# Performance work log

Hardware: AMD Instinct MI355X
Metric: run time of the kernel (lower is better)

## Reference

```python
import jax, jax.numpy as jnp
import numpy as np

MAX_RHO = 12.0
N_THETAS = 16
N_RHOS = 5
G = N_THETAS * N_RHOS          # 80 gaussians
W_NUM = 5                      # weights_num == n_feat -> per-channel conv
OUT_DIM = 80                   # conv_shape = [80, 80]
EPS = 1e-5


def _initial_coords():
    grid_rho = np.linspace(0.0, MAX_RHO, num=N_RHOS + 1)[1:]
    grid_theta = np.linspace(0.0, 2.0 * np.pi, num=N_THETAS + 1)[:-1]
    gr, gt = np.meshgrid(grid_rho, grid_theta, sparse=False)
    return gr.T.flatten().astype(np.float32), gt.T.flatten().astype(np.float32)


def setup_inputs() -> dict:
    key = jax.random.key(0)
    ks = jax.random.split(key, 6)
    B, N, V = 2, 500, 64
    input_feat = jax.random.normal(ks[0], (B, N, V, W_NUM), dtype=jnp.float32)
    rho_coords = jax.random.uniform(ks[1], (B, N, V), dtype=jnp.float32) * MAX_RHO
    theta_coords = jax.random.uniform(ks[2], (B, N, V), dtype=jnp.float32) * (2.0 * np.pi)
    mask = (jax.random.uniform(ks[3], (B, N, V, 1)) > 0.2).astype(jnp.float32)

    mu_r0, mu_t0 = _initial_coords()
    mu_rho = jnp.tile(jnp.asarray(mu_r0)[None, :], (W_NUM, 1))       # [W, G]
    mu_theta = jnp.tile(jnp.asarray(mu_t0)[None, :], (W_NUM, 1))     # [W, G]
    sigma_rho = jnp.full((W_NUM, G), MAX_RHO / 8.0, dtype=jnp.float32)
    sigma_theta = jnp.ones((W_NUM, G), dtype=jnp.float32)

    # VarianceScaling(scale=1, fan_avg, uniform): limit = sqrt(3 / fan_avg)
    limit = np.sqrt(3.0 / ((G + OUT_DIM) / 2.0)).astype(np.float32)
    W_conv = jax.random.uniform(ks[4], (W_NUM, G, OUT_DIM), dtype=jnp.float32,
                                minval=-limit, maxval=limit)
    b_conv = jnp.zeros((W_NUM, OUT_DIM), dtype=jnp.float32)

    return {
        "input_feat": input_feat, "rho_coords": rho_coords,
        "theta_coords": theta_coords, "mask": mask,
        "mu_rho": mu_rho, "mu_theta": mu_theta,
        "sigma_rho": sigma_rho, "sigma_theta": sigma_theta,
        "W_conv": W_conv, "b_conv": b_conv,
        "n_rotations": 16,
    }


def reference(input_feat, rho_coords, theta_coords, mask,
              mu_rho, mu_theta, sigma_rho, sigma_theta,
              W_conv, b_conv, n_rotations):
    # input_feat: [B,N,V,W]; rho/theta: [B,N,V]; mask: [B,N,V,1]
    two_pi = 2.0 * np.pi
    # rho gaussian is rotation-independent -> compute once: [B,N,V,W,G]
    g_rho = jnp.exp(-jnp.square(rho_coords[..., None, None] - mu_rho)
                    / (jnp.square(sigma_rho) + EPS))
    m = mask[..., None]                      # [B,N,V,1,1]

    def one_rotation(k):
        th = jnp.mod(theta_coords + k * (two_pi / n_rotations), two_pi)
        g_th = jnp.exp(-jnp.square(th[..., None, None] - mu_theta)
                       / (jnp.square(sigma_theta) + EPS))    # [B,N,V,W,G]
        gauss = g_rho * g_th * m
        gauss = gauss / (jnp.sum(gauss, axis=2, keepdims=True) + EPS)  # mean over vertices
        # weighted patch aggregation: each weight i sees only feature channel i
        desc = jnp.einsum('bnvwg,bnvw->bnwg', gauss, input_feat)
        return jnp.einsum('bnwg,wgo->bnwo', desc, W_conv) + b_conv     # [B,N,W,O]

    ks = jnp.arange(n_rotations, dtype=jnp.float32)

    def body(carry, k):
        return jnp.maximum(carry, one_rotation(k)), None

    init = one_rotation(ks[0])
    out, _ = jax.lax.scan(body, init, ks[1:])
    return out  # [B, n_samples, weights_num, conv_shape[0]]
```

## Files before the change

kernel.cpp:

```cpp
#include <hip/hip_runtime.h>

#define V 64
#define W 5
#define G 80
#define O 80
#define NROT 16
#define GPAD 104
#define EPSV 1e-5f
#define NLOG2E (-1.4426950408889634f)

#define XSTR 68

using bf16x8 = __attribute__((ext_vector_type(8))) short;
using f32x4  = __attribute__((ext_vector_type(4))) float;

__device__ __forceinline__ unsigned short f2bf(float x) {
    unsigned u = __float_as_uint(x);
    unsigned r = (u + 0x7FFFu + ((u >> 16) & 1u)) >> 16;
    return (unsigned short)r;
}
__device__ __forceinline__ float pick5(float a0, float a1, float a2,
                                       float a3, float a4, int r) {
    float x = (r == 1) ? a1 : a0;
    x = (r == 2) ? a2 : x;
    x = (r == 3) ? a3 : x;
    x = (r == 4) ? a4 : x;
    return x;
}

#if __has_builtin(__builtin_amdgcn_mfma_f32_16x16x32_f16)
typedef _Float16 elem_t;
typedef elem_t efrag __attribute__((ext_vector_type(8)));
#define EMFMA(a, b, c) __builtin_amdgcn_mfma_f32_16x16x32_f16((a), (b), (c), 0, 0, 0)
__device__ __forceinline__ unsigned epack(float a, float b) {
    auto r = __builtin_amdgcn_cvt_pkrtz(a, b);
    return __builtin_bit_cast(unsigned, r);
}
#else
typedef short elem_t;
typedef elem_t efrag __attribute__((ext_vector_type(8)));
#define EMFMA(a, b, c) __builtin_amdgcn_mfma_f32_16x16x32_bf16((a), (b), (c), 0, 0, 0)
__device__ __forceinline__ unsigned epack(float a, float b) {
    return (unsigned)f2bf(a) | ((unsigned)f2bf(b) << 16);
}
#endif

__global__ __launch_bounds__(64) void pack_wc_kernel(
    const float* __restrict__ Wc, unsigned short* __restrict__ wsB)
{
    const int f = blockIdx.x, l = threadIdx.x;
    const int w = f / 15, r = f % 15, ks = r / 5, nt = r % 5;
    const int g0 = ks * 32 + ((l >> 4) << 3);
    const int o  = nt * 16 + (l & 15);
    unsigned short v[8];
    #pragma unroll
    for (int i = 0; i < 8; ++i) {
        int g = g0 + i;
        v[i] = (g < G) ? f2bf(Wc[(w * G + g) * O + o]) : (unsigned short)0;
    }
    *(uint4*)(wsB + ((size_t)f * 64 + l) * 8) = *(const uint4*)v;
}

__global__ __launch_bounds__(320, 6) void conv_kernel(
    const float* __restrict__ feat,
    const float* __restrict__ rho,
    const float* __restrict__ theta,
    const float* __restrict__ mask,
    const float* __restrict__ mu_rho,
    const float* __restrict__ mu_theta,
    const float* __restrict__ sig_rho,
    const float* __restrict__ sig_theta,
    const unsigned short* __restrict__ wsB,
    const float* __restrict__ bc,
    float* __restrict__ out)
{
    __shared__ __align__(16) float s_x[NROT][XSTR];
    __shared__ __align__(16) float s_fT[W][XSTR];
    __shared__ __align__(16) float s_arg[5][XSTR];
    __shared__ __align__(16) unsigned short s_descT[W * NROT * GPAD];
    __shared__ float s_ct[16], s_mt[16], s_shift[8], s_sre[8];

    const int tid = threadIdx.x;
    const int p = blockIdx.x;
    const int g = tid % G;
    const int j = tid / G;

    const float kstep = 0.39269908169872414f;
    const float two_pi = 6.283185307179586f;
    const float inv_two_pi = 0.15915494309189535f;

    {
        int v = tid / 5, w = tid - 5 * (tid / 5);
        s_fT[w][v] = feat[p * V * W + tid];
    }
    {
        int r = tid >> 6, v = tid & 63;
        float mu_r = mu_rho[r * 16];
        float sr   = sig_rho[r * 16];
        float c_r  = NLOG2E / (sr * sr + EPSV);
        float rv   = rho[p * V + v];
        float mk   = (mask[p * V + v] != 0.0f) ? 0.0f : -1e30f;
        float dr = rv - mu_r;
        float av = fmaf(dr * dr, c_r, mk);
        s_arg[r][v] = av;
        float m = av;
        m = fmaxf(m, __shfl_xor(m, 1));
        m = fmaxf(m, __shfl_xor(m, 2));
        m = fmaxf(m, __shfl_xor(m, 4));
        m = fmaxf(m, __shfl_xor(m, 8));
        m = fmaxf(m, __shfl_xor(m, 16));
        m = fmaxf(m, __shfl_xor(m, 32));
        if (v == 0) {
            float sh = fminf(-m, 60.0f);
            s_shift[r] = sh;
            s_sre[r]   = EPSV * __builtin_amdgcn_exp2f(sh);
        }
    }
    if (tid < 16) {
        float st = sig_theta[tid];
        s_ct[tid] = NLOG2E / (st * st + EPSV);
        s_mt[tid] = mu_theta[tid];
    }
    for (int i = tid; i < V * NROT; i += 320) {
        int v = i >> 4, k = i & 15;
        float x = theta[p * V + v] + (float)k * kstep;
        x -= floorf(x * inv_two_pi) * two_pi;
        s_x[k][v] = x;
    }

    const int wchk = 1 + j;
    const int gr = (g >> 4) << 4;
    const int gt = g & 15;
    int pred = (mu_rho  [wchk * G + g] == mu_rho  [g]) &&
               (mu_theta[wchk * G + g] == mu_theta[g]) &&
               (sig_rho [wchk * G + g] == sig_rho [g]) &&
               (sig_theta[wchk * G + g] == sig_theta[g]) &&
               (mu_rho  [g] == mu_rho  [gr]) &&
               (sig_rho [g] == sig_rho [gr]) &&
               (mu_theta[g] == mu_theta[gt]) &&
               (sig_theta[g] == sig_theta[gt]);
    const int uni = __syncthreads_and(pred);

    if (uni) {
        const int ww = tid >> 6;
        const int l  = tid & 63;
        const int lg = l >> 4, lc = l & 15;
        const int v0 = lg << 3;

        efrag a00, a01, a10, a11;
        {
            int w_a = lc / 5, r_a = lc - 5 * (lc / 5);
            float sh = s_shift[r_a];
            const float* ap = &s_arg[r_a][0];
            const float* fp = &s_fT[w_a][0];
            float4 aa = *(const float4*)(ap + v0);
            float4 ab = *(const float4*)(ap + v0 + 4);
            float4 fa = *(const float4*)(fp + v0);
            float4 fb = *(const float4*)(fp + v0 + 4);
            a00 = __builtin_bit_cast(efrag, make_uint4(
                epack(__builtin_amdgcn_exp2f(aa.x + sh) * fa.x,
                      __builtin_amdgcn_exp2f(aa.y + sh) * fa.y),
                epack(__builtin_amdgcn_exp2f(aa.z + sh) * fa.z,
                      __builtin_amdgcn_exp2f(aa.w + sh) * fa.w),
                epack(__builtin_amdgcn_exp2f(ab.x + sh) * fb.x,
                      __builtin_amdgcn_exp2f(ab.y + sh) * fb.y),
                epack(__builtin_amdgcn_exp2f(ab.z + sh) * fb.z,
                      __builtin_amdgcn_exp2f(ab.w + sh) * fb.w)));
            aa = *(const float4*)(ap + 32 + v0);
            ab = *(const float4*)(ap + 32 + v0 + 4);
            fa = *(const float4*)(fp + 32 + v0);
            fb = *(const float4*)(fp + 32 + v0 + 4);
            a01 = __builtin_bit_cast(efrag, make_uint4(
                epack(__builtin_amdgcn_exp2f(aa.x + sh) * fa.x,
                      __builtin_amdgcn_exp2f(aa.y + sh) * fa.y),
                epack(__builtin_amdgcn_exp2f(aa.z + sh) * fa.z,
                      __builtin_amdgcn_exp2f(aa.w + sh) * fa.w),
                epack(__builtin_amdgcn_exp2f(ab.x + sh) * fb.x,
                      __builtin_amdgcn_exp2f(ab.y + sh) * fb.y),
                epack(__builtin_amdgcn_exp2f(ab.z + sh) * fb.z,
                      __builtin_amdgcn_exp2f(ab.w + sh) * fb.w)));
        }
        if (lc < 14) {
            int m = 16 + lc;
            bool wf = (m < 25);
            int w_b = wf ? (m / 5) : 0;
            int r_b = wf ? (m - 5 * (m / 5)) : (lc - 9);
            float sh = s_shift[r_b];
            const float* ap = &s_arg[r_b][0];
            const float* fp = &s_fT[w_b][0];
            float4 aa = *(const float4*)(ap + v0);
            float4 ab = *(const float4*)(ap + v0 + 4);
            float4 fa = *(const float4*)(fp + v0);
            float4 fb = *(const float4*)(fp + v0 + 4);
            if (!wf) { fa = make_float4(1.f,1.f,1.f,1.f); fb = fa; }
            a10 = __builtin_bit_cast(efrag, make_uint4(
                epack(__builtin_amdgcn_exp2f(aa.x + sh) * fa.x,
                      __builtin_amdgcn_exp2f(aa.y + sh) * fa.y),
                epack(__builtin_amdgcn_exp2f(aa.z + sh) * fa.z,
                      __builtin_amdgcn_exp2f(aa.w + sh) * fa.w),
                epack(__builtin_amdgcn_exp2f(ab.x + sh) * fb.x,
                      __builtin_amdgcn_exp2f(ab.y + sh) * fb.y),
                epack(__builtin_amdgcn_exp2f(ab.z + sh) * fb.z,
                      __builtin_amdgcn_exp2f(ab.w + sh) * fb.w)));
            aa = *(const float4*)(ap + 32 + v0);
            ab = *(const float4*)(ap + 32 + v0 + 4);
            fa = *(const float4*)(fp + 32 + v0);
            fb = *(const float4*)(fp + 32 + v0 + 4);
            if (!wf) { fa = make_float4(1.f,1.f,1.f,1.f); fb = fa; }
            a11 = __builtin_bit_cast(efrag, make_uint4(
                epack(__builtin_amdgcn_exp2f(aa.x + sh) * fa.x,
                      __builtin_amdgcn_exp2f(aa.y + sh) * fa.y),
                epack(__builtin_amdgcn_exp2f(aa.z + sh) * fa.z,
                      __builtin_amdgcn_exp2f(aa.w + sh) * fa.w),
                epack(__builtin_amdgcn_exp2f(ab.x + sh) * fb.x,
                      __builtin_amdgcn_exp2f(ab.y + sh) * fb.y),
                epack(__builtin_amdgcn_exp2f(ab.z + sh) * fb.z,
                      __builtin_amdgcn_exp2f(ab.w + sh) * fb.w)));
        } else {
            uint4 zz = make_uint4(0u, 0u, 0u, 0u);
            a10 = __builtin_bit_cast(efrag, zz);
            a11 = __builtin_bit_cast(efrag, zz);
        }

        const float sre0 = s_sre[0], sre1 = s_sre[1], sre2 = s_sre[2],
                    sre3 = s_sre[3], sre4 = s_sre[4];

        int w0[4], r0[4], w1[4], r1[4];
        bool ok1[4];
        #pragma unroll
        for (int i = 0; i < 4; ++i) {
            int m = lg * 4 + i;
            w0[i] = m / 5; r0[i] = m - 5 * w0[i];
            int m2 = 16 + lg * 4 + i;
            ok1[i] = (m2 < 25);
            int mm = ok1[i] ? m2 : 24;
            w1[i] = mm / 5; r1[i] = mm - 5 * w1[i];
        }

        #pragma unroll
        for (int q = 0; q < 4; ++q) {
            int nt = ww + 5 * q;
            if (nt < 16) {
                float ct = s_ct[nt], mt = s_mt[nt];
                float bco = -2.0f * ct * mt;
                float cco = ct * mt * mt;
                const float* xr = &s_x[lc][v0];
                float4 xa = *(const float4*)(xr);
                float4 xb = *(const float4*)(xr + 4);
                float4 xc = *(const float4*)(xr + 32);
                float4 xd = *(const float4*)(xr + 36);
                #define EX(v) __builtin_amdgcn_exp2f(\
                    fmaf(fmaf(ct, (v), bco), (v), cco))
                efrag b0 = __builtin_bit_cast(efrag, make_uint4(
                    epack(EX(xa.x), EX(xa.y)), epack(EX(xa.z), EX(xa.w)),
                    epack(EX(xb.x), EX(xb.y)), epack(EX(xb.z), EX(xb.w))));
                efrag b1 = __builtin_bit_cast(efrag, make_uint4(
                    epack(EX(xc.x), EX(xc.y)), epack(EX(xc.z), EX(xc.w)),
                    epack(EX(xd.x), EX(xd.y)), epack(EX(xd.z), EX(xd.w))));
                #undef EX

                f32x4 z = {0.f, 0.f, 0.f, 0.f};
                f32x4 c0 = EMFMA(a00, b0, z);
                c0 = EMFMA(a01, b1, c0);
                f32x4 c1 = EMFMA(a10, b0, z);
                c1 = EMFMA(a11, b1, c1);

                float dn0 = __shfl(c1[1], 32 + lc);
                float dn1 = __shfl(c1[2], 32 + lc);
                float dn2 = __shfl(c1[3], 32 + lc);
                float dn3 = __shfl(c1[0], 48 + lc);
                float dn4 = __shfl(c1[1], 48 + lc);
                float i0 = __builtin_amdgcn_rcpf(dn0 + sre0);
                float i1 = __builtin_amdgcn_rcpf(dn1 + sre1);
                float i2 = __builtin_amdgcn_rcpf(dn2 + sre2);
                float i3 = __builtin_amdgcn_rcpf(dn3 + sre3);
                float i4 = __builtin_amdgcn_rcpf(dn4 + sre4);

                #pragma unroll
                for (int i = 0; i < 4; ++i) {
                    float inv = pick5(i0, i1, i2, i3, i4, r0[i]);
                    s_descT[(w0[i] * 16 + lc) * GPAD + r0[i] * 16 + nt] =
                        f2bf(c0[i] * inv);
                }
                #pragma unroll
                for (int i = 0; i < 4; ++i) {
                    if (ok1[i]) {
                        float inv = pick5(i0, i1, i2, i3, i4, r1[i]);
                        s_descT[(w1[i] * 16 + lc) * GPAD + r1[i] * 16 + nt] =
                            f2bf(c1[i] * inv);
                    }
                }
            }
        }
    } else {
        #pragma unroll 1
        for (int w = 0; w < W; ++w) {
            const float mu_r = mu_rho[w * G + g];
            const float sr   = sig_rho[w * G + g];
            const float c_sr = NLOG2E / (sr * sr + EPSV);
            const float mu_t = mu_theta[w * G + g];
            const float st   = sig_theta[w * G + g];
            const float c_st = NLOG2E / (st * st + EPSV);
            float den[4] = {0.f, 0.f, 0.f, 0.f};
            float nm[4]  = {0.f, 0.f, 0.f, 0.f};
            for (int v = 0; v < V; ++v) {
                float rv  = rho[p * V + v];
                float mk  = (mask[p * V + v] != 0.0f) ? 0.0f : -1e30f;
                float fw  = s_fT[w][v];
                float dr = rv - mu_r;
                float argr = fmaf(dr * dr, c_sr, mk);
                #pragma unroll
                for (int kk = 0; kk < 4; ++kk) {
                    float x = s_x[4 * j + kk][v];
                    float t = x - mu_t;
                    float e = __builtin_amdgcn_exp2f(fmaf(t * t, c_st, argr));
                    den[kk] += e;
                    nm[kk] = fmaf(e, fw, nm[kk]);
                }
            }
            #pragma unroll
            for (int kk = 0; kk < 4; ++kk)
                s_descT[(w * 16 + 4 * j + kk) * GPAD + g] =
                    f2bf(nm[kk] * __builtin_amdgcn_rcpf(den[kk] + EPSV));
        }
    }

    {
        unsigned* d32 = (unsigned*)s_descT;
        for (int i = tid; i < 80 * 12; i += 320)
            d32[(i / 12) * (GPAD / 2) + 40 + (i % 12)] = 0u;
    }
    __syncthreads();

    {
        const int ww = tid >> 6;
        const int l  = tid & 63;
        bf16x8 afrag[3];
        #pragma unroll
        for (int ks = 0; ks < 3; ++ks)
            afrag[ks] = *(const bf16x8*)(s_descT + (ww * 16 + (l & 15)) * GPAD +
                                         ks * 32 + ((l >> 4) << 3));
        #pragma unroll
        for (int nt = 0; nt < 5; ++nt) {
            f32x4 acc = {0.f, 0.f, 0.f, 0.f};
            #pragma unroll
            for (int ks = 0; ks < 3; ++ks) {
                const unsigned short* bp =
                    wsB + ((size_t)(((ww * 3 + ks) * 5 + nt) * 64 + l)) * 8;
                bf16x8 bfrag = *(const bf16x8*)bp;
                acc = __builtin_amdgcn_mfma_f32_16x16x32_bf16(
                          afrag[ks], bfrag, acc, 0, 0, 0);
            }
            float m1 = fmaxf(fmaxf(acc[0], acc[1]), fmaxf(acc[2], acc[3]));
            m1 = fmaxf(m1, __shfl_xor(m1, 16));
            m1 = fmaxf(m1, __shfl_xor(m1, 32));
            if (l < 16) {
                int oo = nt * 16 + l;
                out[p * (W * O) + ww * O + oo] = m1 + bc[ww * O + oo];
            }
        }
    }
}

extern "C" void kernel_launch(void* const* d_in, const int* in_sizes, int n_in,
                              void* d_out, int out_size, void* d_ws, size_t ws_size,
                              hipStream_t stream) {
    const float* feat      = (const float*)d_in[0];
    const float* rho       = (const float*)d_in[1];
    const float* theta     = (const float*)d_in[2];
    const float* mask      = (const float*)d_in[3];
    const float* mu_rho    = (const float*)d_in[4];
    const float* mu_theta  = (const float*)d_in[5];
    const float* sig_rho   = (const float*)d_in[6];
    const float* sig_theta = (const float*)d_in[7];
    const float* Wc        = (const float*)d_in[8];
    const float* bc        = (const float*)d_in[9];
    float* outp            = (float*)d_out;

    const int np = in_sizes[1] / V;
    unsigned short* ws = (unsigned short*)d_ws;

    pack_wc_kernel<<<75, 64, 0, stream>>>(Wc, ws);
    conv_kernel<<<np, 320, 0, stream>>>(feat, rho, theta, mask, mu_rho, mu_theta,
                                        sig_rho, sig_theta, ws, bc, outp);
}
```

Before: 23.87 us.

## Fuse weight packing into conv kernel and use f16 MFMA for output GEMM

Removes the separate pack_wc_kernel launch. Each conv block now loads W_conv straight from fp32 global memory, converts it to f16 (or bf16) MFMA fragments in registers, and keeps 15 fragments live through the GEMM stage. The descriptor buffer and the final GEMM switch to the same element type as the first stage, f16 when that is available. The launch-bounds occupancy hint drops from 6 to 5 to make room for the extra registers. In exchange, every one of the 1000 blocks re-reads and re-converts the weights with strided loads, and register pressure rises.

```diff
diff --git a/kernel.cpp b/kernel.cpp
--- a/kernel.cpp
+++ b/kernel.cpp
@@ -11,8 +11,7 @@
 
 #define XSTR 68
 
-using bf16x8 = __attribute__((ext_vector_type(8))) short;
-using f32x4  = __attribute__((ext_vector_type(4))) float;
+using f32x4 = __attribute__((ext_vector_type(4))) float;
 
 __device__ __forceinline__ unsigned short f2bf(float x) {
     unsigned u = __float_as_uint(x);
@@ -36,6 +35,7 @@
     auto r = __builtin_amdgcn_cvt_pkrtz(a, b);
     return __builtin_bit_cast(unsigned, r);
 }
+__device__ __forceinline__ elem_t ecast(float x) { return (_Float16)x; }
 #else
 typedef short elem_t;
 typedef elem_t efrag __attribute__((ext_vector_type(8)));
@@ -43,25 +43,10 @@
 __device__ __forceinline__ unsigned epack(float a, float b) {
     return (unsigned)f2bf(a) | ((unsigned)f2bf(b) << 16);
 }
+__device__ __forceinline__ elem_t ecast(float x) { return (elem_t)f2bf(x); }
 #endif
 
-__global__ __launch_bounds__(64) void pack_wc_kernel(
-    const float* __restrict__ Wc, unsigned short* __restrict__ wsB)
-{
-    const int f = blockIdx.x, l = threadIdx.x;
-    const int w = f / 15, r = f % 15, ks = r / 5, nt = r % 5;
-    const int g0 = ks * 32 + ((l >> 4) << 3);
-    const int o  = nt * 16 + (l & 15);
-    unsigned short v[8];
-    #pragma unroll
-    for (int i = 0; i < 8; ++i) {
-        int g = g0 + i;
-        v[i] = (g < G) ? f2bf(Wc[(w * G + g) * O + o]) : (unsigned short)0;
-    }
-    *(uint4*)(wsB + ((size_t)f * 64 + l) * 8) = *(const uint4*)v;
-}
-
-__global__ __launch_bounds__(320, 6) void conv_kernel(
+__global__ __launch_bounds__(320, 5) void conv_kernel(
     const float* __restrict__ feat,
     const float* __restrict__ rho,
     const float* __restrict__ theta,
@@ -70,14 +55,14 @@
     const float* __restrict__ mu_theta,
     const float* __restrict__ sig_rho,
     const float* __restrict__ sig_theta,
-    const unsigned short* __restrict__ wsB,
+    const float* __restrict__ Wc,
     const float* __restrict__ bc,
     float* __restrict__ out)
 {
     __shared__ __align__(16) float s_x[NROT][XSTR];
     __shared__ __align__(16) float s_fT[W][XSTR];
     __shared__ __align__(16) float s_arg[5][XSTR];
-    __shared__ __align__(16) unsigned short s_descT[W * NROT * GPAD];
+    __shared__ __align__(16) elem_t s_descT[W * NROT * GPAD];
     __shared__ float s_ct[16], s_mt[16], s_shift[8], s_sre[8];
 
     const int tid = threadIdx.x;
@@ -141,12 +126,12 @@
                (sig_theta[g] == sig_theta[gt]);
     const int uni = __syncthreads_and(pred);
 
+    const int ww = tid >> 6;
+    const int l  = tid & 63;
+    const int lg = l >> 4, lc = l & 15;
+    const int v0 = lg << 3;
+
     if (uni) {
-        const int ww = tid >> 6;
-        const int l  = tid & 63;
-        const int lg = l >> 4, lc = l & 15;
-        const int v0 = lg << 3;
-
         efrag a00, a01, a10, a11;
         {
             int w_a = lc / 5, r_a = lc - 5 * (lc / 5);
@@ -280,14 +265,14 @@
                 for (int i = 0; i < 4; ++i) {
                     float inv = pick5(i0, i1, i2, i3, i4, r0[i]);
                     s_descT[(w0[i] * 16 + lc) * GPAD + r0[i] * 16 + nt] =
-                        f2bf(c0[i] * inv);
+                        ecast(c0[i] * inv);
                 }
                 #pragma unroll
                 for (int i = 0; i < 4; ++i) {
                     if (ok1[i]) {
                         float inv = pick5(i0, i1, i2, i3, i4, r1[i]);
                         s_descT[(w1[i] * 16 + lc) * GPAD + r1[i] * 16 + nt] =
-                            f2bf(c1[i] * inv);
+                            ecast(c1[i] * inv);
                     }
                 }
             }
@@ -321,7 +306,29 @@
             #pragma unroll
             for (int kk = 0; kk < 4; ++kk)
                 s_descT[(w * 16 + 4 * j + kk) * GPAD + g] =
-                    f2bf(nm[kk] * __builtin_amdgcn_rcpf(den[kk] + EPSV));
+                    ecast(nm[kk] * __builtin_amdgcn_rcpf(den[kk] + EPSV));
+        }
+    }
+
+    efrag bw0[5], bw1[5], bw2[5];
+    {
+        #pragma unroll
+        for (int nt = 0; nt < 5; ++nt) {
+            #pragma unroll
+            for (int ks = 0; ks < 3; ++ks) {
+                int g0 = ks * 32 + lg * 8;
+                const float* wp = Wc + (ww * G + g0) * O + nt * 16 + lc;
+                float v[8];
+                #pragma unroll
+                for (int i = 0; i < 8; ++i)
+                    v[i] = (g0 + i < G) ? wp[i * O] : 0.0f;
+                efrag f = __builtin_bit_cast(efrag, make_uint4(
+                    epack(v[0], v[1]), epack(v[2], v[3]),
+                    epack(v[4], v[5]), epack(v[6], v[7])));
+                if (ks == 0) bw0[nt] = f;
+                else if (ks == 1) bw1[nt] = f;
+                else bw2[nt] = f;
+            }
         }
     }
 
@@ -333,24 +340,17 @@
     __syncthreads();
 
     {
-        const int ww = tid >> 6;
-        const int l  = tid & 63;
-        bf16x8 afrag[3];
+        efrag afrag[3];
         #pragma unroll
         for (int ks = 0; ks < 3; ++ks)
-            afrag[ks] = *(const bf16x8*)(s_descT + (ww * 16 + (l & 15)) * GPAD +
-                                         ks * 32 + ((l >> 4) << 3));
+            afrag[ks] = *(const efrag*)(s_descT + (ww * 16 + lc) * GPAD +
+                                        ks * 32 + (lg << 3));
         #pragma unroll
         for (int nt = 0; nt < 5; ++nt) {
             f32x4 acc = {0.f, 0.f, 0.f, 0.f};
-            #pragma unroll
-            for (int ks = 0; ks < 3; ++ks) {
-                const unsigned short* bp =
-                    wsB + ((size_t)(((ww * 3 + ks) * 5 + nt) * 64 + l)) * 8;
-                bf16x8 bfrag = *(const bf16x8*)bp;
-                acc = __builtin_amdgcn_mfma_f32_16x16x32_bf16(
-                          afrag[ks], bfrag, acc, 0, 0, 0);
-            }
+            acc = EMFMA(afrag[0], bw0[nt], acc);
+            acc = EMFMA(afrag[1], bw1[nt], acc);
+            acc = EMFMA(afrag[2], bw2[nt], acc);
             float m1 = fmaxf(fmaxf(acc[0], acc[1]), fmaxf(acc[2], acc[3]));
             m1 = fmaxf(m1, __shfl_xor(m1, 16));
             m1 = fmaxf(m1, __shfl_xor(m1, 32));
@@ -378,9 +378,6 @@
     float* outp            = (float*)d_out;
 
     const int np = in_sizes[1] / V;
-    unsigned short* ws = (unsigned short*)d_ws;
-
-    pack_wc_kernel<<<75, 64, 0, stream>>>(Wc, ws);
     conv_kernel<<<np, 320, 0, stream>>>(feat, rho, theta, mask, mu_rho, mu_theta,
-                                        sig_rho, sig_theta, ws, bc, outp);
-}
+                                        sig_rho, sig_theta, Wc, bc, outp);
+}
```

New measurement: 53.06 us. 122% more time.
